# Performance work log

Hardware: AMD Instinct MI355X
Metric: run time of the kernel (lower is better)

The kernel has to match this reference:

```python
import jax, jax.numpy as jnp
import numpy as np

DIM = 1024
HID = 2816
E = 8
TOPK = 2
B, S = 4, 1024


def setup_inputs() -> dict:
    key = jax.random.key(0)
    k_x, k_g, k1, k2, k3 = jax.random.split(key, 5)
    scale_d = 1.0 / np.sqrt(DIM)
    scale_h = 1.0 / np.sqrt(HID)
    return {
        "x": jax.random.normal(k_x, (B, S, DIM), dtype=jnp.float32),
        "Wg": jax.random.normal(k_g, (E, DIM), dtype=jnp.float32) * scale_d,   # gate: Linear(dim, E), no bias
        "W1": jax.random.normal(k1, (E, HID, DIM), dtype=jnp.float32) * scale_d,  # swiglu gate proj
        "W3": jax.random.normal(k3, (E, HID, DIM), dtype=jnp.float32) * scale_d,  # swiglu up proj
        "W2": jax.random.normal(k2, (E, DIM, HID), dtype=jnp.float32) * scale_h,  # down proj
    }


def reference(x, Wg, W1, W3, W2):
    Bsz, Ssz, D = x.shape
    xt = x.reshape(Bsz * Ssz, D)                        # [T, D]

    # Gating: top-k over expert scores, softmax over selected logits
    scores = xt @ Wg.T                                   # [T, E]
    top_vals, top_idx = jax.lax.top_k(scores, TOPK)      # [T, K]
    weights = jax.nn.softmax(top_vals, axis=-1)          # [T, K]

    # Dense grouped SwiGLU: run every expert on every token (vectorized),
    # then gather the top-k expert outputs per token.
    h1 = jnp.einsum('td,ehd->teh', xt, W1)               # [T, E, H]
    h3 = jnp.einsum('td,ehd->teh', xt, W3)               # [T, E, H]
    expert_out = jnp.einsum('teh,edh->ted', jax.nn.silu(h1) * h3, W2)  # [T, E, D]

    # Gather per-token selected experts and combine with gate weights
    idx = top_idx[:, :, None]                            # [T, K, 1]
    sel = jnp.take_along_axis(expert_out, idx, axis=1)   # [T, K, D]
    out = jnp.sum(sel * weights[:, :, None], axis=1)     # [T, D]
    return out.reshape(Bsz, Ssz, D)
```

## Files before the change

kernel.cpp:

```cpp
#include <hip/hip_runtime.h>
#include <hip/hip_bf16.h>

#define DIM  1024
#define HID  2816
#define NE   8
#define NTOK 4096
#define NPAIR 8192
#define CAP  8192

#define NT_UPX (HID / 128)
#define NT_DN (DIM / 128)
#define MT    (CAP / 128)
#define NWG_DN (NE * NT_DN * MT)

#define WELEM ((size_t)NE * DIM * HID)

typedef __bf16 bf16x8 __attribute__((ext_vector_type(8)));
typedef float f32x4 __attribute__((ext_vector_type(4)));

#define OFF_CNT  0
#define OFF_LIST 1024
#define OFF_WP   (OFF_LIST + NE*CAP*4)
#define OFF_H1   (OFF_WP + NPAIR*4)
#define OFF_XB   ((size_t)1 << 20)
#define OFF_W1B  ((size_t)10 << 20)
#define OFF_W3B  ((size_t)57 << 20)
#define OFF_H2   ((size_t)106 << 20)
#define WS_NEED  (OFF_H2 + (size_t)NPAIR * HID * 2)
#define OFF_W2B2 ((size_t)153 << 20)
#define WS_BIG   ((size_t)200 << 20)

#define GLB(p) ((const __attribute__((address_space(1))) void*)(p))
#define LDS(p) ((__attribute__((address_space(3))) void*)(p))

__device__ __forceinline__ bf16x8 pack8(float4 a, float4 b) {
  bf16x8 v;
  v[0] = (__bf16)a.x; v[1] = (__bf16)a.y; v[2] = (__bf16)a.z; v[3] = (__bf16)a.w;
  v[4] = (__bf16)b.x; v[5] = (__bf16)b.y; v[6] = (__bf16)b.z; v[7] = (__bf16)b.w;
  return v;
}

__global__ __launch_bounds__(64) void gate_kernel(
    const float* __restrict__ x, const float* __restrict__ Wg,
    int* __restrict__ counts, int* __restrict__ list, float* __restrict__ wpair,
    __bf16* __restrict__ xb) {
  int t = blockIdx.x;
  int lane = threadIdx.x;
  const float* xp = x + (size_t)t * DIM;
  float xr[16];
#pragma unroll
  for (int i = 0; i < 16; ++i) xr[i] = xp[lane + 64 * i];
  if (xb) {
    __bf16* xo = xb + (size_t)t * DIM;
#pragma unroll
    for (int i = 0; i < 16; ++i) xo[lane + 64 * i] = (__bf16)xr[i];
  }
  float s[NE];
#pragma unroll
  for (int e = 0; e < NE; ++e) {
    const float* wp = Wg + e * DIM;
    float acc = 0.f;
#pragma unroll
    for (int i = 0; i < 16; ++i) acc += xr[i] * wp[lane + 64 * i];
#pragma unroll
    for (int off = 32; off >= 1; off >>= 1) acc += __shfl_xor(acc, off, 64);
    s[e] = acc;
  }
  if (lane == 0) {
    int i0 = 0; float b0 = s[0];
#pragma unroll
    for (int e = 1; e < NE; ++e) if (s[e] > b0) { b0 = s[e]; i0 = e; }
    int i1 = -1; float b1 = -1e30f;
#pragma unroll
    for (int e = 0; e < NE; ++e) if (e != i0 && s[e] > b1) { b1 = s[e]; i1 = e; }
    float e1 = __expf(b1 - b0);
    float w0 = 1.f / (1.f + e1);
    float w1 = e1 * w0;
    int s0 = atomicAdd(&counts[i0], 1);
    list[i0 * CAP + s0] = 2 * t;
    wpair[2 * t] = w0;
    int s1 = atomicAdd(&counts[i1], 1);
    list[i1 * CAP + s1] = 2 * t + 1;
    wpair[2 * t + 1] = w1;
  }
}

__global__ __launch_bounds__(256) void cvt16_kernel(
    const float* __restrict__ src, __bf16* __restrict__ dst) {
  size_t i = (((size_t)blockIdx.x * 256) + threadIdx.x) * 16;
  float4 f0 = *(const float4*)(src + i);
  float4 f1 = *(const float4*)(src + i + 4);
  float4 f2 = *(const float4*)(src + i + 8);
  float4 f3 = *(const float4*)(src + i + 12);
  *(bf16x8*)(dst + i)     = pack8(f0, f1);
  *(bf16x8*)(dst + i + 8) = pack8(f2, f3);
}

__global__ __launch_bounds__(256, 2) void up10_kernel(
    const __bf16* __restrict__ xb, const __bf16* __restrict__ w1b,
    const __bf16* __restrict__ w3b, const int* __restrict__ counts,
    const int* __restrict__ list, const float* __restrict__ wpair,
    __bf16* __restrict__ Hbuf, const float* __restrict__ W2,
    __bf16* __restrict__ w2b) {
  if (blockIdx.x >= NT_UPX) {
    int c = (blockIdx.x - NT_UPX) + 2 * (blockIdx.y + 64 * blockIdx.z);
    size_t base = (size_t)c * 22528;
    int tid = threadIdx.x;
#pragma unroll
    for (int i = 0; i < 11; ++i) {
      size_t off = base + (size_t)i * 2048 + (size_t)tid * 8;
      float4 f0 = *(const float4*)(W2 + off);
      float4 f1 = *(const float4*)(W2 + off + 4);
      *(bf16x8*)(w2b + off) = pack8(f0, f1);
    }
    return;
  }

  int e = blockIdx.z;
  int cnt = counts[e];
  int m0 = blockIdx.y * 128;
  if (m0 >= cnt) return;
  int h0 = blockIdx.x * 128;

  __shared__ __bf16 As[128 * 64];
  __shared__ __bf16 B1s[128 * 64];
  __shared__ __bf16 B3s[128 * 64];

  int tid = threadIdx.x;
  int lane = tid & 63;
  int w = tid >> 6;
  int cl = lane & 15, hi = lane >> 4;
  int wr = w >> 1, wc = w & 1;
  int l8 = lane >> 3, cc = lane & 7;

  const __bf16* asrc[4];
  const __bf16* b1src[4];
  const __bf16* b3src[4];
#pragma unroll
  for (int i = 0; i < 4; ++i) {
    int r = (w * 4 + i) * 8 + l8;
    int csel = (cc ^ (r & 7)) * 8;
    int mrow = m0 + r; if (mrow > cnt - 1) mrow = cnt - 1;
    int p = list[e * CAP + mrow];
    asrc[i]  = xb + (size_t)(p >> 1) * DIM + csel;
    b1src[i] = w1b + ((size_t)e * HID + h0 + r) * DIM + csel;
    b3src[i] = w3b + ((size_t)e * HID + h0 + r) * DIM + csel;
  }

  f32x4 acc1[4][4] = {};
  f32x4 acc3[4][4] = {};

  for (int k0 = 0; k0 < DIM; k0 += 64) {
#pragma unroll
    for (int i = 0; i < 4; ++i) {
      int q = (w * 4 + i) * 1024;
      __builtin_amdgcn_global_load_lds(GLB(asrc[i] + k0),  LDS((char*)As  + q), 16, 0, 0);
      __builtin_amdgcn_global_load_lds(GLB(b1src[i] + k0), LDS((char*)B1s + q), 16, 0, 0);
      __builtin_amdgcn_global_load_lds(GLB(b3src[i] + k0), LDS((char*)B3s + q), 16, 0, 0);
    }
    __syncthreads();
#pragma unroll
    for (int ks = 0; ks < 2; ++ks) {
      int c = hi + ks * 4;
      bf16x8 a[4], bb1[4], bb3[4];
#pragma unroll
      for (int mi = 0; mi < 4; ++mi) {
        int r = wr * 64 + mi * 16 + cl;
        a[mi] = *(const bf16x8*)((const char*)As + r * 128 + ((c ^ (r & 7)) * 16));
      }
#pragma unroll
      for (int ni = 0; ni < 4; ++ni) {
        int r = wc * 64 + ni * 16 + cl;
        bb1[ni] = *(const bf16x8*)((const char*)B1s + r * 128 + ((c ^ (r & 7)) * 16));
        bb3[ni] = *(const bf16x8*)((const char*)B3s + r * 128 + ((c ^ (r & 7)) * 16));
      }
#pragma unroll
      for (int mi = 0; mi < 4; ++mi)
#pragma unroll
        for (int ni = 0; ni < 4; ++ni) {
          acc1[mi][ni] = __builtin_amdgcn_mfma_f32_16x16x32_bf16(a[mi], bb1[ni], acc1[mi][ni], 0, 0, 0);
          acc3[mi][ni] = __builtin_amdgcn_mfma_f32_16x16x32_bf16(a[mi], bb3[ni], acc3[mi][ni], 0, 0, 0);
        }
    }
    __syncthreads();
  }

#pragma unroll
  for (int mi = 0; mi < 4; ++mi) {
#pragma unroll
    for (int rr = 0; rr < 4; ++rr) {
      int m = m0 + wr * 64 + mi * 16 + hi * 4 + rr;
      if (m < cnt) {
        int p = list[e * CAP + m];
        float wgt = wpair[p];
        __bf16* hp = Hbuf + (size_t)p * HID + h0 + wc * 64 + cl;
#pragma unroll
        for (int ni = 0; ni < 4; ++ni) {
          float v1 = acc1[mi][ni][rr], v3 = acc3[mi][ni][rr];
          float gv = (v1 / (1.f + __expf(-v1))) * v3 * wgt;
          hp[ni * 16] = (__bf16)gv;
        }
      }
    }
  }
}

__global__ __launch_bounds__(256, 2) void down9_kernel(
    const __bf16* __restrict__ Hbuf, const __bf16* __restrict__ w2b,
    const int* __restrict__ counts, const int* __restrict__ list,
    __bf16* __restrict__ Obuf) {
  int bid = blockIdx.x;
  int g = (bid & 7) * (NWG_DN / 8) + (bid >> 3);
  int e = g / (NT_DN * MT);
  int rr0 = g % (NT_DN * MT);
  int cnt = counts[e];
  int m0 = (rr0 % MT) * 128;
  if (m0 >= cnt) return;
  int d0 = (rr0 / MT) * 128;

  __shared__ __bf16 As[128 * 64];
  __shared__ __bf16 Bs[128 * 64];

  int tid = threadIdx.x;
  int lane = tid & 63;
  int w = tid >> 6;
  int cl = lane & 15, hi = lane >> 4;
  int wr = w >> 1, wc = w & 1;
  int l8 = lane >> 3, cc = lane & 7;

  const __bf16* asrc[4];
  const __bf16* bsrc[4];
#pragma unroll
  for (int i = 0; i < 4; ++i) {
    int r = (w * 4 + i) * 8 + l8;
    int csel = (cc ^ (r & 7)) * 8;
    int mrow = m0 + r; if (mrow > cnt - 1) mrow = cnt - 1;
    int p = list[e * CAP + mrow];
    asrc[i] = Hbuf + (size_t)p * HID + csel;
    bsrc[i] = w2b + ((size_t)e * DIM + d0 + r) * HID + csel;
  }

  f32x4 acc[4][4] = {};

  for (int k0 = 0; k0 < HID; k0 += 64) {
#pragma unroll
    for (int i = 0; i < 4; ++i) {
      int q = (w * 4 + i) * 1024;
      __builtin_amdgcn_global_load_lds(GLB(asrc[i] + k0), LDS((char*)As + q), 16, 0, 0);
      __builtin_amdgcn_global_load_lds(GLB(bsrc[i] + k0), LDS((char*)Bs + q), 16, 0, 0);
    }
    __syncthreads();
#pragma unroll
    for (int ks = 0; ks < 2; ++ks) {
      int c = hi + ks * 4;
      bf16x8 a[4], b[4];
#pragma unroll
      for (int mi = 0; mi < 4; ++mi) {
        int r = wr * 64 + mi * 16 + cl;
        a[mi] = *(const bf16x8*)((const char*)As + r * 128 + ((c ^ (r & 7)) * 16));
      }
#pragma unroll
      for (int ni = 0; ni < 4; ++ni) {
        int r = wc * 64 + ni * 16 + cl;
        b[ni] = *(const bf16x8*)((const char*)Bs + r * 128 + ((c ^ (r & 7)) * 16));
      }
#pragma unroll
      for (int mi = 0; mi < 4; ++mi)
#pragma unroll
        for (int ni = 0; ni < 4; ++ni)
          acc[mi][ni] = __builtin_amdgcn_mfma_f32_16x16x32_bf16(a[mi], b[ni], acc[mi][ni], 0, 0, 0);
    }
    __syncthreads();
  }

#pragma unroll
  for (int mi = 0; mi < 4; ++mi) {
#pragma unroll
    for (int rr = 0; rr < 4; ++rr) {
      int m = m0 + wr * 64 + mi * 16 + hi * 4 + rr;
      if (m < cnt) {
        int p = list[e * CAP + m];
        __bf16* op = Obuf + (size_t)p * DIM + d0 + wc * 64 + cl;
#pragma unroll
        for (int ni = 0; ni < 4; ++ni)
          op[ni * 16] = (__bf16)acc[mi][ni][rr];
      }
    }
  }
}

__global__ __launch_bounds__(256) void combine_kernel(
    const __bf16* __restrict__ Obuf, float* __restrict__ out) {
  size_t j = (((size_t)blockIdx.x * 256) + threadIdx.x) * 8;
  size_t t = j >> 10;
  bf16x8 a = *(const bf16x8*)(Obuf + j + t * DIM);
  bf16x8 b = *(const bf16x8*)(Obuf + j + t * DIM + DIM);
  float4 o0, o1;
  o0.x = (float)a[0] + (float)b[0]; o0.y = (float)a[1] + (float)b[1];
  o0.z = (float)a[2] + (float)b[2]; o0.w = (float)a[3] + (float)b[3];
  o1.x = (float)a[4] + (float)b[4]; o1.y = (float)a[5] + (float)b[5];
  o1.z = (float)a[6] + (float)b[6]; o1.w = (float)a[7] + (float)b[7];
  *(float4*)(out + j) = o0;
  *(float4*)(out + j + 4) = o1;
}

__device__ __forceinline__ void cvt_store16(__bf16* dst, const float* src) {
#pragma unroll
  for (int j = 0; j < 2; ++j) {
    float4 f0 = *(const float4*)(src + j * 8);
    float4 f1 = *(const float4*)(src + j * 8 + 4);
    *(bf16x8*)(dst + j * 8) = pack8(f0, f1);
  }
}

__global__ __launch_bounds__(256) void up_kernel(
    const float* __restrict__ x, const float* __restrict__ W1,
    const float* __restrict__ W3, const int* __restrict__ counts,
    const int* __restrict__ list, __bf16* __restrict__ Hbuf) {
  int e = blockIdx.z;
  int cnt = counts[e];
  int m0 = blockIdx.y * 64;
  if (m0 >= cnt) return;
  int h0 = blockIdx.x * 64;

  __shared__ __bf16 As[64][72];
  __shared__ __bf16 B1s[64][72];
  __shared__ __bf16 B3s[64][72];

  int tid = threadIdx.x;
  int r = tid >> 2;
  int cs = (tid & 3) * 16;

  const float* asrc = nullptr;
  int mrow = m0 + r;
  if (mrow < cnt) {
    int p = list[e * CAP + mrow];
    asrc = x + (size_t)(p >> 1) * DIM;
  }
  const float* b1src = W1 + ((size_t)e * HID + (h0 + r)) * DIM;
  const float* b3src = W3 + ((size_t)e * HID + (h0 + r)) * DIM;

  int lane = tid & 63;
  int w = tid >> 6;
  int wr = w >> 1, wc = w & 1;
  int cl = lane & 15, hi = lane >> 4;

  f32x4 acc1[2][2] = {};
  f32x4 acc3[2][2] = {};

  for (int k0 = 0; k0 < DIM; k0 += 64) {
    if (asrc) {
      cvt_store16(&As[r][cs], asrc + k0 + cs);
    } else {
      bf16x8 z = {};
      *(bf16x8*)&As[r][cs] = z;
      *(bf16x8*)&As[r][cs + 8] = z;
    }
    cvt_store16(&B1s[r][cs], b1src + k0 + cs);
    cvt_store16(&B3s[r][cs], b3src + k0 + cs);
    __syncthreads();
#pragma unroll
    for (int ks = 0; ks < 64; ks += 32) {
      bf16x8 a[2], b1f[2], b3f[2];
#pragma unroll
      for (int mi = 0; mi < 2; ++mi)
        a[mi] = *(const bf16x8*)&As[wr * 32 + mi * 16 + cl][ks + hi * 8];
#pragma unroll
      for (int ni = 0; ni < 2; ++ni) {
        b1f[ni] = *(const bf16x8*)&B1s[wc * 32 + ni * 16 + cl][ks + hi * 8];
        b3f[ni] = *(const bf16x8*)&B3s[wc * 32 + ni * 16 + cl][ks + hi * 8];
      }
#pragma unroll
      for (int mi = 0; mi < 2; ++mi)
#pragma unroll
        for (int ni = 0; ni < 2; ++ni) {
          acc1[mi][ni] = __builtin_amdgcn_mfma_f32_16x16x32_bf16(a[mi], b1f[ni], acc1[mi][ni], 0, 0, 0);
          acc3[mi][ni] = __builtin_amdgcn_mfma_f32_16x16x32_bf16(a[mi], b3f[ni], acc3[mi][ni], 0, 0, 0);
        }
    }
    __syncthreads();
  }

#pragma unroll
  for (int mi = 0; mi < 2; ++mi) {
#pragma unroll
    for (int rr = 0; rr < 4; ++rr) {
      int m = m0 + wr * 32 + mi * 16 + hi * 4 + rr;
      if (m < cnt) {
        int p = list[e * CAP + m];
        __bf16* hp = Hbuf + (size_t)p * HID + h0 + wc * 32 + cl;
#pragma unroll
        for (int ni = 0; ni < 2; ++ni) {
          float v1 = acc1[mi][ni][rr], v3 = acc3[mi][ni][rr];
          float gg = (v1 / (1.f + __expf(-v1))) * v3;
          hp[ni * 16] = (__bf16)gg;
        }
      }
    }
  }
}

__global__ __launch_bounds__(256) void down_kernel(
    const __bf16* __restrict__ Hbuf, const float* __restrict__ W2,
    const int* __restrict__ counts, const int* __restrict__ list,
    const float* __restrict__ wpair, float* __restrict__ out) {
  int e = blockIdx.z;
  int cnt = counts[e];
  int m0 = blockIdx.y * 64;
  if (m0 >= cnt) return;
  int d0 = blockIdx.x * 64;

  __shared__ __bf16 As[64][72];
  __shared__ __bf16 Bs[64][72];

  int tid = threadIdx.x;
  int r = tid >> 2;
  int cs = (tid & 3) * 16;

  const __bf16* asrc = nullptr;
  int mrow = m0 + r;
  if (mrow < cnt) {
    int p = list[e * CAP + mrow];
    asrc = Hbuf + (size_t)p * HID;
  }
  const float* bsrc = W2 + ((size_t)e * DIM + (d0 + r)) * HID;

  int lane = tid & 63;
  int w = tid >> 6;
  int wr = w >> 1, wc = w & 1;
  int cl = lane & 15, hi = lane >> 4;

  f32x4 acc[2][2] = {};

  for (int k0 = 0; k0 < HID; k0 += 64) {
    if (asrc) {
      *(bf16x8*)&As[r][cs]     = *(const bf16x8*)(asrc + k0 + cs);
      *(bf16x8*)&As[r][cs + 8] = *(const bf16x8*)(asrc + k0 + cs + 8);
    } else {
      bf16x8 z = {};
      *(bf16x8*)&As[r][cs] = z;
      *(bf16x8*)&As[r][cs + 8] = z;
    }
    cvt_store16(&Bs[r][cs], bsrc + k0 + cs);
    __syncthreads();
#pragma unroll
    for (int ks = 0; ks < 64; ks += 32) {
      bf16x8 a[2], b[2];
#pragma unroll
      for (int mi = 0; mi < 2; ++mi)
        a[mi] = *(const bf16x8*)&As[wr * 32 + mi * 16 + cl][ks + hi * 8];
#pragma unroll
      for (int ni = 0; ni < 2; ++ni)
        b[ni] = *(const bf16x8*)&Bs[wc * 32 + ni * 16 + cl][ks + hi * 8];
#pragma unroll
      for (int mi = 0; mi < 2; ++mi)
#pragma unroll
        for (int ni = 0; ni < 2; ++ni)
          acc[mi][ni] = __builtin_amdgcn_mfma_f32_16x16x32_bf16(a[mi], b[ni], acc[mi][ni], 0, 0, 0);
    }
    __syncthreads();
  }

#pragma unroll
  for (int mi = 0; mi < 2; ++mi) {
#pragma unroll
    for (int rr = 0; rr < 4; ++rr) {
      int m = m0 + wr * 32 + mi * 16 + hi * 4 + rr;
      if (m < cnt) {
        int p = list[e * CAP + m];
        int t = p >> 1;
        float wgt = wpair[p];
        float* op = out + (size_t)t * DIM + d0 + wc * 32 + cl;
#pragma unroll
        for (int ni = 0; ni < 2; ++ni)
          atomicAdd(&op[ni * 16], wgt * acc[mi][ni][rr]);
      }
    }
  }
}

extern "C" void kernel_launch(void* const* d_in, const int* in_sizes, int n_in,
                              void* d_out, int out_size, void* d_ws, size_t ws_size,
                              hipStream_t stream) {
  const float* x  = (const float*)d_in[0];
  const float* Wg = (const float*)d_in[1];
  const float* W1 = (const float*)d_in[2];
  const float* W3 = (const float*)d_in[3];
  const float* W2 = (const float*)d_in[4];
  float* out = (float*)d_out;

  char* ws = (char*)d_ws;
  int* counts  = (int*)(ws + OFF_CNT);
  int* list    = (int*)(ws + OFF_LIST);
  float* wpair = (float*)(ws + OFF_WP);

  hipMemsetAsync(counts, 0, 64, stream);

  if (ws_size >= WS_NEED) {
    __bf16* xb   = (__bf16*)(ws + OFF_XB);
    __bf16* w1b  = (__bf16*)(ws + OFF_W1B);
    __bf16* w3b  = (__bf16*)(ws + OFF_W3B);
    __bf16* Hbuf = (__bf16*)(ws + OFF_H2);
    __bf16* Obuf = (__bf16*)(ws + OFF_W3B);

    gate_kernel<<<NTOK, 64, 0, stream>>>(x, Wg, counts, list, wpair, xb);

    cvt16_kernel<<<WELEM / 4096, 256, 0, stream>>>(W1, w1b);
    cvt16_kernel<<<WELEM / 4096, 256, 0, stream>>>(W3, w3b);

    if (ws_size >= WS_BIG) {
      __bf16* w2b = (__bf16*)(ws + OFF_W2B2);
      up10_kernel<<<dim3(NT_UPX + 2, CAP / 128, NE), 256, 0, stream>>>(
          xb, w1b, w3b, counts, list, wpair, Hbuf, W2, w2b);
      down9_kernel<<<NWG_DN, 256, 0, stream>>>(Hbuf, w2b, counts, list, Obuf);
    } else {
      up10_kernel<<<dim3(NT_UPX, CAP / 128, NE), 256, 0, stream>>>(
          xb, w1b, w3b, counts, list, wpair, Hbuf, W2, nullptr);
      cvt16_kernel<<<WELEM / 4096, 256, 0, stream>>>(W2, w1b);
      down9_kernel<<<NWG_DN, 256, 0, stream>>>(Hbuf, w1b, counts, list, Obuf);
    }

    combine_kernel<<<NTOK * DIM / 2048, 256, 0, stream>>>(Obuf, out);
  } else {
    hipMemsetAsync(d_out, 0, (size_t)out_size * sizeof(float), stream);
    __bf16* Hbuf = (__bf16*)(ws + OFF_H1);
    gate_kernel<<<NTOK, 64, 0, stream>>>(x, Wg, counts, list, wpair, nullptr);
    up_kernel<<<dim3(HID / 64, CAP / 64, NE), 256, 0, stream>>>(x, W1, W3, counts, list, Hbuf);
    down_kernel<<<dim3(DIM / 64, CAP / 64, NE), 256, 0, stream>>>(Hbuf, W2, counts, list, wpair, out);
  }
}
```

Baseline: 383.8 us.

## Split down-projection K dimension in two and sum partial slabs in combine

The down-projection GEMM now splits the HID reduction into two halves, launching twice as many workgroups, each writing its partial result to a separate Obuf slab. The combine kernel reads both slabs for both top-k pairs and sums them. The weight conversion kernel is also changed to handle 8 elements per thread with twice the grid. The goal is more parallelism and better occupancy in the down GEMM, at the cost of extra partial-output writes and reads plus a second bf16 rounding of the partials. The Obuf region overlaps w3b, so the second slab must fit in that workspace.

Measured after the change: 388.6 us. About the same (+1.2%).

```diff
diff --git a/kernel.cpp b/kernel.cpp
--- a/kernel.cpp
+++ b/kernel.cpp
@@ -11,7 +11,9 @@
 #define NT_UPX (HID / 128)
 #define NT_DN (DIM / 128)
 #define MT    (CAP / 128)
-#define NWG_DN (NE * NT_DN * MT)
+#define KHALF (HID / 2)
+#define NWG_DN2 (NE * NT_DN * 2 * MT)
+#define SLAB  ((size_t)NPAIR * DIM)
 
 #define WELEM ((size_t)NE * DIM * HID)
 
@@ -85,15 +87,12 @@
   }
 }
 
-__global__ __launch_bounds__(256) void cvt16_kernel(
+__global__ __launch_bounds__(256) void cvt_kernel(
     const float* __restrict__ src, __bf16* __restrict__ dst) {
-  size_t i = (((size_t)blockIdx.x * 256) + threadIdx.x) * 16;
+  size_t i = (((size_t)blockIdx.x * 256) + threadIdx.x) * 8;
   float4 f0 = *(const float4*)(src + i);
   float4 f1 = *(const float4*)(src + i + 4);
-  float4 f2 = *(const float4*)(src + i + 8);
-  float4 f3 = *(const float4*)(src + i + 12);
-  *(bf16x8*)(dst + i)     = pack8(f0, f1);
-  *(bf16x8*)(dst + i + 8) = pack8(f2, f3);
+  *(bf16x8*)(dst + i) = pack8(f0, f1);
 }
 
 __global__ __launch_bounds__(256, 2) void up10_kernel(
@@ -205,18 +204,23 @@
   }
 }
 
-__global__ __launch_bounds__(256, 2) void down9_kernel(
+__global__ __launch_bounds__(256, 2) void down11_kernel(
     const __bf16* __restrict__ Hbuf, const __bf16* __restrict__ w2b,
     const int* __restrict__ counts, const int* __restrict__ list,
     __bf16* __restrict__ Obuf) {
   int bid = blockIdx.x;
-  int g = (bid & 7) * (NWG_DN / 8) + (bid >> 3);
-  int e = g / (NT_DN * MT);
-  int rr0 = g % (NT_DN * MT);
+  int g = (bid & 7) * (NWG_DN2 / 8) + (bid >> 3);
+  int mt = g % MT;
+  int q  = g / MT;
+  int s  = q & 1;
+  int q2 = q >> 1;
+  int nt = q2 & 7;
+  int e  = q2 >> 3;
   int cnt = counts[e];
-  int m0 = (rr0 % MT) * 128;
+  int m0 = mt * 128;
   if (m0 >= cnt) return;
-  int d0 = (rr0 / MT) * 128;
+  int d0 = nt * 128;
+  int kbase = s * KHALF;
 
   __shared__ __bf16 As[128 * 64];
   __shared__ __bf16 Bs[128 * 64];
@@ -242,12 +246,12 @@
 
   f32x4 acc[4][4] = {};
 
-  for (int k0 = 0; k0 < HID; k0 += 64) {
+  for (int k0 = kbase; k0 < kbase + KHALF; k0 += 64) {
 #pragma unroll
     for (int i = 0; i < 4; ++i) {
-      int q = (w * 4 + i) * 1024;
-      __builtin_amdgcn_global_load_lds(GLB(asrc[i] + k0), LDS((char*)As + q), 16, 0, 0);
-      __builtin_amdgcn_global_load_lds(GLB(bsrc[i] + k0), LDS((char*)Bs + q), 16, 0, 0);
+      int q8 = (w * 4 + i) * 1024;
+      __builtin_amdgcn_global_load_lds(GLB(asrc[i] + k0), LDS((char*)As + q8), 16, 0, 0);
+      __builtin_amdgcn_global_load_lds(GLB(bsrc[i] + k0), LDS((char*)Bs + q8), 16, 0, 0);
     }
     __syncthreads();
 #pragma unroll
@@ -280,7 +284,7 @@
       int m = m0 + wr * 64 + mi * 16 + hi * 4 + rr;
       if (m < cnt) {
         int p = list[e * CAP + m];
-        __bf16* op = Obuf + (size_t)p * DIM + d0 + wc * 64 + cl;
+        __bf16* op = Obuf + (size_t)s * SLAB + (size_t)p * DIM + d0 + wc * 64 + cl;
 #pragma unroll
         for (int ni = 0; ni < 4; ++ni)
           op[ni * 16] = (__bf16)acc[mi][ni][rr];
@@ -289,19 +293,20 @@
   }
 }
 
-__global__ __launch_bounds__(256) void combine_kernel(
+__global__ __launch_bounds__(256) void combine2_kernel(
     const __bf16* __restrict__ Obuf, float* __restrict__ out) {
   size_t j = (((size_t)blockIdx.x * 256) + threadIdx.x) * 8;
   size_t t = j >> 10;
-  bf16x8 a = *(const bf16x8*)(Obuf + j + t * DIM);
-  bf16x8 b = *(const bf16x8*)(Obuf + j + t * DIM + DIM);
-  float4 o0, o1;
-  o0.x = (float)a[0] + (float)b[0]; o0.y = (float)a[1] + (float)b[1];
-  o0.z = (float)a[2] + (float)b[2]; o0.w = (float)a[3] + (float)b[3];
-  o1.x = (float)a[4] + (float)b[4]; o1.y = (float)a[5] + (float)b[5];
-  o1.z = (float)a[6] + (float)b[6]; o1.w = (float)a[7] + (float)b[7];
-  *(float4*)(out + j) = o0;
-  *(float4*)(out + j + 4) = o1;
+  bf16x8 a0 = *(const bf16x8*)(Obuf + j + t * DIM);
+  bf16x8 b0 = *(const bf16x8*)(Obuf + j + t * DIM + DIM);
+  bf16x8 a1 = *(const bf16x8*)(Obuf + SLAB + j + t * DIM);
+  bf16x8 b1 = *(const bf16x8*)(Obuf + SLAB + j + t * DIM + DIM);
+  float o[8];
+#pragma unroll
+  for (int i = 0; i < 8; ++i)
+    o[i] = ((float)a0[i] + (float)a1[i]) + ((float)b0[i] + (float)b1[i]);
+  *(float4*)(out + j)     = make_float4(o[0], o[1], o[2], o[3]);
+  *(float4*)(out + j + 4) = make_float4(o[4], o[5], o[6], o[7]);
 }
 
 __device__ __forceinline__ void cvt_store16(__bf16* dst, const float* src) {
@@ -505,22 +510,22 @@
 
     gate_kernel<<<NTOK, 64, 0, stream>>>(x, Wg, counts, list, wpair, xb);
 
-    cvt16_kernel<<<WELEM / 4096, 256, 0, stream>>>(W1, w1b);
-    cvt16_kernel<<<WELEM / 4096, 256, 0, stream>>>(W3, w3b);
+    cvt_kernel<<<WELEM / 2048, 256, 0, stream>>>(W1, w1b);
+    cvt_kernel<<<WELEM / 2048, 256, 0, stream>>>(W3, w3b);
 
     if (ws_size >= WS_BIG) {
       __bf16* w2b = (__bf16*)(ws + OFF_W2B2);
       up10_kernel<<<dim3(NT_UPX + 2, CAP / 128, NE), 256, 0, stream>>>(
           xb, w1b, w3b, counts, list, wpair, Hbuf, W2, w2b);
-      down9_kernel<<<NWG_DN, 256, 0, stream>>>(Hbuf, w2b, counts, list, Obuf);
+      down11_kernel<<<NWG_DN2, 256, 0, stream>>>(Hbuf, w2b, counts, list, Obuf);
     } else {
       up10_kernel<<<dim3(NT_UPX, CAP / 128, NE), 256, 0, stream>>>(
           xb, w1b, w3b, counts, list, wpair, Hbuf, W2, nullptr);
-      cvt16_kernel<<<WELEM / 4096, 256, 0, stream>>>(W2, w1b);
-      down9_kernel<<<NWG_DN, 256, 0, stream>>>(Hbuf, w1b, counts, list, Obuf);
-    }
-
-    combine_kernel<<<NTOK * DIM / 2048, 256, 0, stream>>>(Obuf, out);
+      cvt_kernel<<<WELEM / 2048, 256, 0, stream>>>(W2, w1b);
+      down11_kernel<<<NWG_DN2, 256, 0, stream>>>(Hbuf, w1b, counts, list, Obuf);
+    }
+
+    combine2_kernel<<<NTOK * DIM / 2048, 256, 0, stream>>>(Obuf, out);
   } else {
     hipMemsetAsync(d_out, 0, (size_t)out_size * sizeof(float), stream);
     __bf16* Hbuf = (__bf16*)(ws + OFF_H1);
```
